# Optimization experiments

Measured on AMD Instinct MI355X. Metric: run time of the kernel, lower is better.

Reference implementation:

```python
import jax, jax.numpy as jnp
import numpy as np

N_CHILDS = 50000
N_EDGES = 500000
NODE_FEAT = 256
NUM_SEM = 57
HID = 256
EDGE_FEAT = 64
EDGE_TYPES = 4
NUM_ITERS = 2


def setup_inputs() -> dict:
    key = jax.random.key(0)
    ks = jax.random.split(key, 12)
    d_in = NODE_FEAT + NUM_SEM            # 313
    d_ne = 2 * HID + EDGE_FEAT + EDGE_TYPES  # 580
    d_par = HID * (NUM_ITERS + 1)         # 768
    def lin(k, fan_in, fan_out):
        kw, kb = jax.random.split(k)
        s = 1.0 / np.sqrt(fan_in)
        return (jax.random.uniform(kw, (fan_in, fan_out), jnp.float32, -s, s),
                jax.random.uniform(kb, (fan_out,), jnp.float32, -s, s))
    W_child, b_child = lin(ks[0], d_in, HID)
    W_ne0, b_ne0 = lin(ks[1], d_ne, HID)
    W_ne1, b_ne1 = lin(ks[2], d_ne, HID)
    W_parent, b_parent = lin(ks[3], d_par, NODE_FEAT)
    return {
        "child_feats": jax.random.normal(ks[4], (1, N_CHILDS, d_in), jnp.float32),
        "child_exists": jnp.ones((1, N_CHILDS, 1), jnp.float32),
        "edge_type_onehot": jax.random.normal(ks[5], (1, N_EDGES, EDGE_TYPES), jnp.float32),
        "edge_feats": jax.random.normal(ks[6], (1, N_EDGES, EDGE_FEAT), jnp.float32),
        "edge_indices": jax.random.randint(ks[7], (1, N_EDGES, 2), 0, N_CHILDS, jnp.int64),
        "W_child": W_child, "b_child": b_child,
        "W_ne0": W_ne0, "b_ne0": b_ne0,
        "W_ne1": W_ne1, "b_ne1": b_ne1,
        "W_parent": W_parent, "b_parent": b_parent,
    }


def reference(child_feats, child_exists, edge_type_onehot, edge_feats, edge_indices,
              W_child, b_child, W_ne0, b_ne0, W_ne1, b_ne1, W_parent, b_parent):
    n = child_feats.shape[1]
    # node embedding: linear + relu, mask non-existent children
    x = jax.nn.relu(jnp.einsum('bnd,dh->bnh', child_feats, W_child) + b_child)
    x = x * child_exists                              # [1, N, H]
    iter_parent = [x.max(axis=1)]                     # symmetric_type == 'max'
    ef = jnp.concatenate([edge_type_onehot, edge_feats], axis=2)[0]  # [E, 4+64]
    src = edge_indices[0, :, 0]
    dst = edge_indices[0, :, 1]
    cnt = jax.ops.segment_sum(jnp.ones((src.shape[0],), x.dtype), src, num_segments=n)
    denom = jnp.maximum(cnt, 1.0)[:, None]            # scatter_mean clamp
    for W, b in ((W_ne0, b_ne0), (W_ne1, b_ne1)):
        nef = jnp.concatenate([x[0, src], x[0, dst], ef], axis=1)  # [E, 580]
        nef = jax.nn.relu(nef @ W + b)                # [E, H]
        # edge_symmetric_type == 'avg': scatter_mean over source index
        x = (jax.ops.segment_sum(nef, src, num_segments=n) / denom)[None]
        iter_parent.append(x.max(axis=1))
    parent = jnp.concatenate(iter_parent, axis=1)     # [1, H*(iters+1)]
    return jax.nn.relu(parent @ W_parent + b_parent)  # [1, node_feat_size]
```

## Files before the change

### kernel.cpp

```cpp
#include <hip/hip_runtime.h>

#define NC   50000
#define NE   500000
#define DIN  313
#define DNE  580
#define KPC  320
#define KB   96
#define NB_SCAN 196

typedef __attribute__((ext_vector_type(8))) short bf16x8;
typedef __attribute__((ext_vector_type(4))) float f32x4;

static __device__ __forceinline__ unsigned short f2bf(float f) {
    unsigned u = __float_as_uint(f);
    unsigned r = (u + 0x7fff + ((u >> 16) & 1)) >> 16;
    return (unsigned short)r;
}
static __device__ __forceinline__ float bf2f(unsigned short u) {
    return __uint_as_float(((unsigned)u) << 16);
}
static __device__ __forceinline__ void gload_lds16(const unsigned short* g, unsigned short* l) {
    __builtin_amdgcn_global_load_lds(
        (const __attribute__((address_space(1))) unsigned int*)(g),
        (__attribute__((address_space(3))) unsigned int*)(l), 16, 0, 0);
}

__global__ __launch_bounds__(256) void prep_w_kernel(
    const float* __restrict__ W0, const float* __restrict__ W1,
    const float* __restrict__ Wc,
    unsigned short* __restrict__ Wpt, unsigned short* __restrict__ Wbt,
    unsigned short* __restrict__ Wct)
{
    int b = blockIdx.x;
    if (b < 1024) {
        int layer = b >> 9, n2 = b & 511;
        const float* W = layer ? W1 : W0;
        unsigned short* dst = Wpt + (size_t)layer * 512 * 256 + (size_t)n2 * 256;
        int t = threadIdx.x;
        int ch = t >> 5, s = (t >> 3) & 3, j = t & 7;
        int gk = ch * 32 + ((s ^ (n2 & 3)) * 8) + j;
        float v = (n2 < 256) ? W[(size_t)gk * 256 + n2] : W[(size_t)(256 + gk) * 256 + (n2 - 256)];
        dst[t] = f2bf(v);
    } else if (b < 1536) {
        int idx = b - 1024;
        int layer = idx >> 8, n = idx & 255;
        const float* W = layer ? W1 : W0;
        unsigned short* dst = Wbt + (size_t)layer * 256 * KB + (size_t)n * KB;
        int t = threadIdx.x;
        if (t < KB) {
            float v = (512 + t < DNE) ? W[(size_t)(512 + t) * 256 + n] : 0.0f;
            dst[t] = f2bf(v);
        }
    } else {
        int n = b - 1536;
        unsigned short* dst = Wct + (size_t)n * KPC;
        for (int t = threadIdx.x; t < KPC; t += 256) {
            int ch = t >> 5, s = (t >> 3) & 3, j = t & 7;
            int gk = ch * 32 + ((s ^ (n & 3)) * 8) + j;
            float v = (gk < DIN) ? Wc[(size_t)gk * 256 + n] : 0.0f;
            dst[t] = f2bf(v);
        }
    }
}

__global__ __launch_bounds__(256, 4) void child_mfma_kernel(
    const float* __restrict__ cf, const float* __restrict__ exists,
    const unsigned short* __restrict__ Wct, const float* __restrict__ bias,
    unsigned short* __restrict__ xb, float* __restrict__ pmax)
{
    __shared__ unsigned short sA[64][40];
    __shared__ unsigned short sB[256][32];
    __shared__ float smax[256];

    const int tid = threadIdx.x, lane = tid & 63, wid = tid >> 6;
    const int wm = wid >> 1, wn = wid & 1, l15 = lane & 15, l4 = lane >> 4;
    const int node0 = blockIdx.x * 64;
    const int arow = tid >> 2, s3 = tid & 3;

    smax[tid] = 0.0f;

    f32x4 acc[2][8];
    #pragma unroll
    for (int mi = 0; mi < 2; ++mi)
        #pragma unroll
        for (int ni = 0; ni < 8; ++ni)
            acc[mi][ni] = (f32x4){0.f, 0.f, 0.f, 0.f};

    int nodeA = node0 + arow; if (nodeA >= NC) nodeA = NC - 1;

    for (int ch = 0; ch < 10; ++ch) {
        #pragma unroll
        for (int i = 0; i < 4; ++i) {
            int n = (wid << 6) + (i << 4) + (lane >> 2);
            gload_lds16(Wct + (size_t)n * KPC + ch * 32 + (lane & 3) * 8,
                        &sB[(wid << 6) + (i << 4)][0]);
        }
        {
            int gk0 = ch * 32 + s3 * 8;
            union { unsigned short u[8]; int4 v; } pk;
            #pragma unroll
            for (int j = 0; j < 8; ++j) {
                int gk = gk0 + j;
                float f = (gk < DIN) ? cf[(size_t)nodeA * DIN + gk] : 0.0f;
                pk.u[j] = f2bf(f);
            }
            *(int4*)&sA[arow][s3 * 8] = pk.v;
        }
        __syncthreads();
        bf16x8 af[2];
        #pragma unroll
        for (int mi = 0; mi < 2; ++mi)
            af[mi] = *(const bf16x8*)&sA[wm * 32 + mi * 16 + l15][l4 * 8];
        #pragma unroll
        for (int ni = 0; ni < 8; ++ni) {
            int n = wn * 128 + ni * 16 + l15;
            bf16x8 bfr = *(const bf16x8*)&sB[n][(l4 ^ (n & 3)) * 8];
            acc[0][ni] = __builtin_amdgcn_mfma_f32_16x16x32_bf16(af[0], bfr, acc[0][ni], 0, 0, 0);
            acc[1][ni] = __builtin_amdgcn_mfma_f32_16x16x32_bf16(af[1], bfr, acc[1][ni], 0, 0, 0);
        }
        __syncthreads();
    }

    float bv[8];
    #pragma unroll
    for (int ni = 0; ni < 8; ++ni) bv[ni] = bias[wn * 128 + ni * 16 + l15];
    float cmax[8];
    #pragma unroll
    for (int ni = 0; ni < 8; ++ni) cmax[ni] = 0.0f;

    #pragma unroll
    for (int mi = 0; mi < 2; ++mi) {
        #pragma unroll
        for (int r = 0; r < 4; ++r) {
            int node = node0 + wm * 32 + mi * 16 + l4 * 4 + r;
            if (node < NC) {
                float ex = exists[node];
                #pragma unroll
                for (int ni = 0; ni < 8; ++ni) {
                    float v = fmaxf(acc[mi][ni][r] + bv[ni], 0.f) * ex;
                    xb[(size_t)node * 256 + wn * 128 + ni * 16 + l15] = f2bf(v);
                    cmax[ni] = fmaxf(cmax[ni], v);
                }
            }
        }
    }
    #pragma unroll
    for (int ni = 0; ni < 8; ++ni)
        atomicMax((unsigned int*)&smax[wn * 128 + ni * 16 + l15], __float_as_uint(cmax[ni]));
    __syncthreads();
    atomicMax((unsigned int*)&pmax[tid], __float_as_uint(smax[tid]));
}

__global__ __launch_bounds__(256, 3) void node_gemm_kernel(
    const unsigned short* __restrict__ xb,
    const unsigned short* __restrict__ Wpt,
    unsigned short* __restrict__ yp)
{
    __shared__ unsigned short sA[2][64][40];
    __shared__ unsigned short sB[2][256][32];

    const int tid = threadIdx.x, lane = tid & 63, wid = tid >> 6;
    const int wm = wid >> 1, wn = wid & 1, l15 = lane & 15, l4 = lane >> 4;
    const int node0 = blockIdx.x * 64;
    const int n0 = blockIdx.y * 256;
    const int arow = tid >> 2, s3 = tid & 3;

    int nodeA = node0 + arow; if (nodeA >= NC) nodeA = NC - 1;

    f32x4 acc[2][8];
    #pragma unroll
    for (int mi = 0; mi < 2; ++mi)
        #pragma unroll
        for (int ni = 0; ni < 8; ++ni)
            acc[mi][ni] = (f32x4){0.f, 0.f, 0.f, 0.f};

    #pragma unroll
    for (int i = 0; i < 4; ++i) {
        int n = (wid << 6) + (i << 4) + (lane >> 2);
        gload_lds16(Wpt + (size_t)(n0 + n) * 256 + (lane & 3) * 8, &sB[0][(wid << 6) + (i << 4)][0]);
    }
    *(int4*)&sA[0][arow][s3 * 8] = *(const int4*)(xb + (size_t)nodeA * 256 + s3 * 8);
    __syncthreads();

    int buf = 0;
    for (int ch = 0; ch < 8; ++ch) {
        const int nch = ch + 1;
        int4 areg;
        if (nch < 8) {
            #pragma unroll
            for (int i = 0; i < 4; ++i) {
                int n = (wid << 6) + (i << 4) + (lane >> 2);
                gload_lds16(Wpt + (size_t)(n0 + n) * 256 + nch * 32 + (lane & 3) * 8,
                            &sB[buf ^ 1][(wid << 6) + (i << 4)][0]);
            }
            areg = *(const int4*)(xb + (size_t)nodeA * 256 + nch * 32 + s3 * 8);
        }
        bf16x8 af[2];
        #pragma unroll
        for (int mi = 0; mi < 2; ++mi)
            af[mi] = *(const bf16x8*)&sA[buf][wm * 32 + mi * 16 + l15][l4 * 8];
        #pragma unroll
        for (int ni = 0; ni < 8; ++ni) {
            int n = wn * 128 + ni * 16 + l15;
            bf16x8 bfr = *(const bf16x8*)&sB[buf][n][(l4 ^ (n & 3)) * 8];
            acc[0][ni] = __builtin_amdgcn_mfma_f32_16x16x32_bf16(af[0], bfr, acc[0][ni], 0, 0, 0);
            acc[1][ni] = __builtin_amdgcn_mfma_f32_16x16x32_bf16(af[1], bfr, acc[1][ni], 0, 0, 0);
        }
        if (nch < 8) *(int4*)&sA[buf ^ 1][arow][s3 * 8] = areg;
        __syncthreads();
        buf ^= 1;
    }

    #pragma unroll
    for (int mi = 0; mi < 2; ++mi) {
        #pragma unroll
        for (int r = 0; r < 4; ++r) {
            int node = node0 + wm * 32 + mi * 16 + l4 * 4 + r;
            if (node < NC) {
                #pragma unroll
                for (int ni = 0; ni < 8; ++ni)
                    yp[(size_t)node * 512 + n0 + wn * 128 + ni * 16 + l15] = f2bf(acc[mi][ni][r]);
            }
        }
    }
}

__global__ __launch_bounds__(256) void count_int_kernel(
    const int* __restrict__ eidx, int* __restrict__ icnt)
{
    int t = blockIdx.x * 256 + threadIdx.x;
    if (t < NE) atomicAdd(&icnt[eidx[2 * t]], 1);
}

__global__ __launch_bounds__(256) void scan1_kernel(
    const int* __restrict__ icnt, int* __restrict__ part)
{
    __shared__ int sd[256];
    int i = blockIdx.x * 256 + threadIdx.x;
    sd[threadIdx.x] = (i < NC) ? icnt[i] : 0;
    __syncthreads();
    for (int d = 128; d > 0; d >>= 1) {
        if (threadIdx.x < d) sd[threadIdx.x] += sd[threadIdx.x + d];
        __syncthreads();
    }
    if (threadIdx.x == 0) part[blockIdx.x] = sd[0];
}

__global__ void scan2_kernel(int* __restrict__ part)
{
    if (threadIdx.x == 0) {
        int acc = 0;
        for (int i = 0; i < NB_SCAN; ++i) { int v = part[i]; part[i] = acc; acc += v; }
    }
}

__global__ __launch_bounds__(256) void scan3_kernel(
    const int* __restrict__ icnt, const int* __restrict__ part,
    int* __restrict__ cur)
{
    __shared__ int sc[256];
    const int t = threadIdx.x;
    int i = blockIdx.x * 256 + t;
    int val = (i < NC) ? icnt[i] : 0;
    sc[t] = val;
    __syncthreads();
    for (int d = 1; d < 256; d <<= 1) {
        int x = (t >= d) ? sc[t - d] : 0;
        __syncthreads();
        sc[t] += x;
        __syncthreads();
    }
    if (i < NC) cur[i] = part[blockIdx.x] + sc[t] - val;
}

__global__ __launch_bounds__(256) void bin_kernel(
    const int* __restrict__ eidx, int* __restrict__ cur, int* __restrict__ perm)
{
    int t = blockIdx.x * 256 + threadIdx.x;
    if (t < NE) {
        int s = eidx[2 * t];
        int p = atomicAdd(&cur[s], 1);
        perm[p] = t;
    }
}

__global__ __launch_bounds__(256) void inv_kernel(
    const int* __restrict__ icnt, float* __restrict__ inv)
{
    int t = blockIdx.x * 256 + threadIdx.x;
    if (t < NC) inv[t] = 1.0f / fmaxf((float)icnt[t], 1.0f);
}

__global__ __launch_bounds__(256, 4) void combine_kernel(
    const unsigned short* __restrict__ yp,
    const float* __restrict__ eto, const float* __restrict__ efe,
    const int* __restrict__ eidx, const int* __restrict__ perm,
    const unsigned short* __restrict__ Wbt,
    const float* __restrict__ bias,
    float* __restrict__ accb)
{
    __shared__ __align__(16) unsigned char smemraw[16 * 258 * 4];
    unsigned short (*sA)[64][40] = (unsigned short (*)[64][40])smemraw;
    float (*ep)[258] = (float (*)[258])smemraw;
    __shared__ int s_src[64], s_dst[64], s_perm[64];

    const int tid = threadIdx.x;
    const int nwg = gridDim.x;
    const int q = nwg >> 3, rr = nwg & 7;
    const int xcd = blockIdx.x & 7, within = blockIdx.x >> 3;
    const int bid = (xcd < rr ? xcd * (q + 1) : rr * (q + 1) + (xcd - rr) * q) + within;
    const int e0 = bid * 64;

    if (tid < 64) {
        int ee = e0 + tid; if (ee >= NE) ee = NE - 1;
        int e = perm[ee];
        s_perm[tid] = e;
        s_src[tid] = eidx[2 * e];
        s_dst[tid] = eidx[2 * e + 1];
    }
    const int lane = tid & 63;
    const int wid  = tid >> 6;
    const int wm   = wid >> 1;
    const int wn   = wid & 1;
    const int l15  = lane & 15;
    const int l4   = lane >> 4;
    const int arow = tid >> 2;
    const int s3   = tid & 3;

    __syncthreads();

    const int my_e = s_perm[arow];
    #pragma unroll
    for (int ch = 0; ch < 3; ++ch) {
        int g0 = ch * 32 + s3 * 8;
        union { unsigned short u[8]; int4 v; } pk;
        #pragma unroll
        for (int j = 0; j < 8; ++j) {
            int g = g0 + j;
            float f = 0.0f;
            if (g < 4)       f = eto[(size_t)my_e * 4 + g];
            else if (g < 68) f = efe[(size_t)my_e * 64 + (g - 4)];
            pk.u[j] = f2bf(f);
        }
        *(int4*)&sA[ch][arow][s3 * 8] = pk.v;
    }
    __syncthreads();

    f32x4 acc[2][8];
    #pragma unroll
    for (int mi = 0; mi < 2; ++mi)
        #pragma unroll
        for (int ni = 0; ni < 8; ++ni)
            acc[mi][ni] = (f32x4){0.f, 0.f, 0.f, 0.f};

    const unsigned short* wp = Wbt + (size_t)(wn * 128 + l15) * KB + l4 * 8;
    #pragma unroll
    for (int ch = 0; ch < 3; ++ch) {
        bf16x8 bw[8];
        #pragma unroll
        for (int ni = 0; ni < 8; ++ni)
            bw[ni] = *(const bf16x8*)(wp + (size_t)ni * 16 * KB + ch * 32);
        bf16x8 af0 = *(const bf16x8*)&sA[ch][wm * 32 + l15][l4 * 8];
        bf16x8 af1 = *(const bf16x8*)&sA[ch][wm * 32 + 16 + l15][l4 * 8];
        #pragma unroll
        for (int ni = 0; ni < 8; ++ni) {
            acc[0][ni] = __builtin_amdgcn_mfma_f32_16x16x32_bf16(af0, bw[ni], acc[0][ni], 0, 0, 0);
            acc[1][ni] = __builtin_amdgcn_mfma_f32_16x16x32_bf16(af1, bw[ni], acc[1][ni], 0, 0, 0);
        }
    }
    __syncthreads();

    const int col = tid;
    const float b_col = bias[col];

    int curn = s_src[0];
    int rstart = 0;
    float run = 0.f;
    #pragma unroll
    for (int c = 0; c < 4; ++c) {
        if (wm == (c >> 1)) {
            const int mi = c & 1;
            #pragma unroll
            for (int ni = 0; ni < 8; ++ni) {
                #pragma unroll
                for (int r = 0; r < 4; ++r)
                    ep[l4 * 4 + r][wn * 128 + ni * 16 + l15] = acc[mi][ni][r];
            }
        }
        float yt[16], ym[16];
        #pragma unroll
        for (int r = 0; r < 16; ++r) {
            int row = c * 16 + r;
            yt[r] = bf2f(yp[(size_t)s_src[row] * 512 + col]);
            ym[r] = bf2f(yp[(size_t)s_dst[row] * 512 + 256 + col]);
        }
        __syncthreads();
        #pragma unroll
        for (int r = 0; r < 16; ++r) {
            int row = c * 16 + r;
            float v = 0.0f;
            if (e0 + row < NE)
                v = fmaxf(ep[r][col] + yt[r] + ym[r] + b_col, 0.f);
            int sr = s_src[row];
            if (sr != curn) {
                if (rstart > 0) accb[(size_t)curn * 256 + col] = run;
                else            atomicAdd(&accb[(size_t)curn * 256 + col], run);
                curn = sr; run = v; rstart = row;
            } else {
                run += v;
            }
        }
        __syncthreads();
    }
    atomicAdd(&accb[(size_t)curn * 256 + col], run);
}

__global__ __launch_bounds__(256) void finalize_kernel(
    const float* __restrict__ src, const float* __restrict__ inv,
    unsigned short* __restrict__ xb_out, float* __restrict__ pmax, int n)
{
    const int tid = threadIdx.x;
    int i0 = blockIdx.x * 128;
    int iend = i0 + 128; if (iend > n) iend = n;
    float m = 0.0f;
    for (int i = i0; i < iend; ++i) {
        float v = src[(size_t)i * 256 + tid];
        v *= inv[i];
        xb_out[(size_t)i * 256 + tid] = f2bf(v);
        m = fmaxf(m, v);
    }
    atomicMax((unsigned int*)&pmax[tid], __float_as_uint(m));
}

__global__ __launch_bounds__(256) void parent_kernel(
    const float* __restrict__ pmax, const float* __restrict__ W,
    const float* __restrict__ bias, float* __restrict__ out)
{
    __shared__ float sp[768];
    const int tid = threadIdx.x;
    for (int i = tid; i < 768; i += 256) sp[i] = pmax[i];
    __syncthreads();
    float s = bias[tid];
    for (int k = 0; k < 768; ++k) s = fmaf(sp[k], W[(size_t)k * 256 + tid], s);
    out[tid] = fmaxf(s, 0.f);
}

extern "C" void kernel_launch(void* const* d_in, const int* in_sizes, int n_in,
                              void* d_out, int out_size, void* d_ws, size_t ws_size,
                              hipStream_t stream)
{
    const float* cf   = (const float*)d_in[0];
    const float* ex   = (const float*)d_in[1];
    const float* eto  = (const float*)d_in[2];
    const float* efe  = (const float*)d_in[3];
    const int*   eidx = (const int*)d_in[4];
    const float* Wc   = (const float*)d_in[5];
    const float* bc   = (const float*)d_in[6];
    const float* W0   = (const float*)d_in[7];
    const float* b0   = (const float*)d_in[8];
    const float* W1   = (const float*)d_in[9];
    const float* b1   = (const float*)d_in[10];
    const float* Wp   = (const float*)d_in[11];
    const float* bp   = (const float*)d_in[12];

    float*          accb = (float*)d_ws;
    float*          invv = accb + (size_t)NC * 256;
    float*          pmax = invv + NC;
    unsigned short* xb   = (unsigned short*)(pmax + 768);
    unsigned short* yp   = xb + (size_t)NC * 256;
    unsigned short* Wpt  = yp + (size_t)NC * 512;
    unsigned short* Wbt  = Wpt + (size_t)2 * 512 * 256;
    unsigned short* Wct  = Wbt + (size_t)2 * 256 * KB;
    int*            icnt = (int*)(Wct + (size_t)256 * KPC);
    int*            part = icnt + NC;
    int*            curb = part + 256;
    int*            perm = curb + NC;

    hipMemsetAsync(pmax, 0, 768 * sizeof(float), stream);
    hipMemsetAsync(icnt, 0, NC * sizeof(int), stream);

    prep_w_kernel<<<1792, 256, 0, stream>>>(W0, W1, Wc, Wpt, Wbt, Wct);
    child_mfma_kernel<<<(NC + 63) / 64, 256, 0, stream>>>(cf, ex, Wct, bc, xb, pmax);

    count_int_kernel<<<(NE + 255) / 256, 256, 0, stream>>>(eidx, icnt);
    scan1_kernel<<<NB_SCAN, 256, 0, stream>>>(icnt, part);
    scan2_kernel<<<1, 64, 0, stream>>>(part);
    scan3_kernel<<<NB_SCAN, 256, 0, stream>>>(icnt, part, curb);
    bin_kernel<<<(NE + 255) / 256, 256, 0, stream>>>(eidx, curb, perm);
    inv_kernel<<<(NC + 255) / 256, 256, 0, stream>>>(icnt, invv);

    for (int it = 0; it < 2; ++it) {
        node_gemm_kernel<<<dim3((NC + 63) / 64, 2), 256, 0, stream>>>(
            xb, Wpt + (size_t)it * 512 * 256, yp);
        hipMemsetAsync(accb, 0, (size_t)NC * 256 * sizeof(float), stream);
        combine_kernel<<<(NE + 63) / 64, 256, 0, stream>>>(
            yp, eto, efe, eidx, perm, Wbt + (size_t)it * 256 * KB, it ? b1 : b0, accb);
        finalize_kernel<<<(NC + 127) / 128, 256, 0, stream>>>(accb, invv, xb, pmax + 256 * (it + 1), NC);
    }
    parent_kernel<<<1, 256, 0, stream>>>(pmax, Wp, bp, (float*)d_out);
}
```

Baseline: 720.8 us.

## Fuse edge combine with node finalize using node-partitioned CSR segments

Edges are now processed per block of 32 destination nodes using CSR offsets, so each block owns complete segments. It can divide by the count and write bf16 node features directly, which removes the fp32 accumulator, its memset, the atomics and the separate finalize kernel. Edge features are precomputed once into sorted, bf16-packed arrays that are loaded with direct-to-LDS loads. The cost is uneven work per block from variable degrees and a serial tile loop per block.

```diff
diff --git a/kernel.cpp b/kernel.cpp
--- a/kernel.cpp
+++ b/kernel.cpp
@@ -2,10 +2,12 @@
 
 #define NC   50000
 #define NE   500000
+#define NEP  (NE + 64)
 #define DIN  313
 #define DNE  580
 #define KPC  320
 #define KB   96
+#define NPB  32
 #define NB_SCAN 196
 
 typedef __attribute__((ext_vector_type(8))) short bf16x8;
@@ -256,7 +258,7 @@
 
 __global__ __launch_bounds__(256) void scan3_kernel(
     const int* __restrict__ icnt, const int* __restrict__ part,
-    int* __restrict__ cur)
+    int* __restrict__ cur, int* __restrict__ soff)
 {
     __shared__ int sc[256];
     const int t = threadIdx.x;
@@ -270,7 +272,11 @@
         sc[t] += x;
         __syncthreads();
     }
-    if (i < NC) cur[i] = part[blockIdx.x] + sc[t] - val;
+    if (i < NC) {
+        int start = part[blockIdx.x] + sc[t] - val;
+        cur[i]  = start;
+        soff[i] = start;
+    }
 }
 
 __global__ __launch_bounds__(256) void bin_kernel(
@@ -285,151 +291,194 @@
 }
 
 __global__ __launch_bounds__(256) void inv_kernel(
-    const int* __restrict__ icnt, float* __restrict__ inv)
+    const int* __restrict__ icnt, float* __restrict__ inv, int* __restrict__ soff)
 {
     int t = blockIdx.x * 256 + threadIdx.x;
     if (t < NC) inv[t] = 1.0f / fmaxf((float)icnt[t], 1.0f);
-}
-
-__global__ __launch_bounds__(256, 4) void combine_kernel(
+    if (blockIdx.x == 0 && threadIdx.x == 0) soff[NC] = NE;
+}
+
+__global__ __launch_bounds__(256) void ef_prep_kernel(
+    const float* __restrict__ eto, const float* __restrict__ efe,
+    const int* __restrict__ perm, const int* __restrict__ eidx,
+    unsigned short* __restrict__ efc01, unsigned short* __restrict__ efc2,
+    int* __restrict__ esrc, int* __restrict__ edst)
+{
+    int p = blockIdx.x * 256 + threadIdx.x;
+    if (p >= NE) return;
+    int e = perm[p];
+    esrc[p] = eidx[2 * e];
+    edst[p] = eidx[2 * e + 1];
+    const float* efr = efe + (size_t)e * 64;
+
+    union { unsigned short u[8]; int4 v; } pk;
+    {
+        float4 a = *(const float4*)(eto + (size_t)e * 4);
+        float4 b = *(const float4*)(efr + 0);
+        pk.u[0]=f2bf(a.x); pk.u[1]=f2bf(a.y); pk.u[2]=f2bf(a.z); pk.u[3]=f2bf(a.w);
+        pk.u[4]=f2bf(b.x); pk.u[5]=f2bf(b.y); pk.u[6]=f2bf(b.z); pk.u[7]=f2bf(b.w);
+        *(int4*)(efc01 + (size_t)p * 32) = pk.v;
+    }
+    #pragma unroll
+    for (int g = 1; g < 4; ++g) {
+        float4 a = *(const float4*)(efr + g * 8 - 4);
+        float4 b = *(const float4*)(efr + g * 8);
+        pk.u[0]=f2bf(a.x); pk.u[1]=f2bf(a.y); pk.u[2]=f2bf(a.z); pk.u[3]=f2bf(a.w);
+        pk.u[4]=f2bf(b.x); pk.u[5]=f2bf(b.y); pk.u[6]=f2bf(b.z); pk.u[7]=f2bf(b.w);
+        *(int4*)(efc01 + (size_t)p * 32 + g * 8) = pk.v;
+    }
+    #pragma unroll
+    for (int g = 0; g < 4; ++g) {
+        float4 a = *(const float4*)(efr + 28 + g * 8);
+        float4 b = *(const float4*)(efr + 32 + g * 8);
+        pk.u[0]=f2bf(a.x); pk.u[1]=f2bf(a.y); pk.u[2]=f2bf(a.z); pk.u[3]=f2bf(a.w);
+        pk.u[4]=f2bf(b.x); pk.u[5]=f2bf(b.y); pk.u[6]=f2bf(b.z); pk.u[7]=f2bf(b.w);
+        *(int4*)(efc01 + ((size_t)NEP + p) * 32 + g * 8) = pk.v;
+    }
+    {
+        float4 a = *(const float4*)(efr + 60);
+        pk.u[0]=f2bf(a.x); pk.u[1]=f2bf(a.y); pk.u[2]=f2bf(a.z); pk.u[3]=f2bf(a.w);
+        pk.u[4]=0; pk.u[5]=0; pk.u[6]=0; pk.u[7]=0;
+        *(int4*)(efc2 + (size_t)p * 8) = pk.v;
+    }
+}
+
+__global__ __launch_bounds__(256, 4) void combine_node_kernel(
     const unsigned short* __restrict__ yp,
-    const float* __restrict__ eto, const float* __restrict__ efe,
-    const int* __restrict__ eidx, const int* __restrict__ perm,
+    const unsigned short* __restrict__ efc01,
+    const unsigned short* __restrict__ efc2,
+    const int* __restrict__ esrc, const int* __restrict__ edst,
+    const int* __restrict__ soff, const float* __restrict__ invv,
     const unsigned short* __restrict__ Wbt,
     const float* __restrict__ bias,
-    float* __restrict__ accb)
-{
-    __shared__ __align__(16) unsigned char smemraw[16 * 258 * 4];
-    unsigned short (*sA)[64][40] = (unsigned short (*)[64][40])smemraw;
-    float (*ep)[258] = (float (*)[258])smemraw;
-    __shared__ int s_src[64], s_dst[64], s_perm[64];
+    unsigned short* __restrict__ xb_out, float* __restrict__ pmax)
+{
+    __shared__ unsigned short sA[2][64][32];
+    __shared__ unsigned short sA2[64][8];
+    __shared__ float ep[16][258];
+    __shared__ int s_src[64], s_dst[64];
+    __shared__ float s_inv[NPB];
+    __shared__ int s_offa[NPB + 1];
 
     const int tid = threadIdx.x;
-    const int nwg = gridDim.x;
-    const int q = nwg >> 3, rr = nwg & 7;
-    const int xcd = blockIdx.x & 7, within = blockIdx.x >> 3;
-    const int bid = (xcd < rr ? xcd * (q + 1) : rr * (q + 1) + (xcd - rr) * q) + within;
-    const int e0 = bid * 64;
-
-    if (tid < 64) {
-        int ee = e0 + tid; if (ee >= NE) ee = NE - 1;
-        int e = perm[ee];
-        s_perm[tid] = e;
-        s_src[tid] = eidx[2 * e];
-        s_dst[tid] = eidx[2 * e + 1];
-    }
-    const int lane = tid & 63;
-    const int wid  = tid >> 6;
-    const int wm   = wid >> 1;
-    const int wn   = wid & 1;
-    const int l15  = lane & 15;
-    const int l4   = lane >> 4;
-    const int arow = tid >> 2;
-    const int s3   = tid & 3;
-
+    const int n0 = blockIdx.x * NPB;
+    if (tid < NPB) {
+        int n = n0 + tid;
+        s_inv[tid] = invv[n < NC ? n : NC - 1];
+    }
+    if (tid <= NPB) {
+        int n = n0 + tid;
+        s_offa[tid] = soff[n < NC ? n : NC];
+    }
     __syncthreads();
-
-    const int my_e = s_perm[arow];
-    #pragma unroll
-    for (int ch = 0; ch < 3; ++ch) {
-        int g0 = ch * 32 + s3 * 8;
-        union { unsigned short u[8]; int4 v; } pk;
-        #pragma unroll
-        for (int j = 0; j < 8; ++j) {
-            int g = g0 + j;
-            float f = 0.0f;
-            if (g < 4)       f = eto[(size_t)my_e * 4 + g];
-            else if (g < 68) f = efe[(size_t)my_e * 64 + (g - 4)];
-            pk.u[j] = f2bf(f);
-        }
-        *(int4*)&sA[ch][arow][s3 * 8] = pk.v;
-    }
-    __syncthreads();
-
-    f32x4 acc[2][8];
-    #pragma unroll
-    for (int mi = 0; mi < 2; ++mi)
-        #pragma unroll
-        for (int ni = 0; ni < 8; ++ni)
-            acc[mi][ni] = (f32x4){0.f, 0.f, 0.f, 0.f};
-
-    const unsigned short* wp = Wbt + (size_t)(wn * 128 + l15) * KB + l4 * 8;
-    #pragma unroll
-    for (int ch = 0; ch < 3; ++ch) {
-        bf16x8 bw[8];
-        #pragma unroll
-        for (int ni = 0; ni < 8; ++ni)
-            bw[ni] = *(const bf16x8*)(wp + (size_t)ni * 16 * KB + ch * 32);
-        bf16x8 af0 = *(const bf16x8*)&sA[ch][wm * 32 + l15][l4 * 8];
-        bf16x8 af1 = *(const bf16x8*)&sA[ch][wm * 32 + 16 + l15][l4 * 8];
-        #pragma unroll
-        for (int ni = 0; ni < 8; ++ni) {
-            acc[0][ni] = __builtin_amdgcn_mfma_f32_16x16x32_bf16(af0, bw[ni], acc[0][ni], 0, 0, 0);
-            acc[1][ni] = __builtin_amdgcn_mfma_f32_16x16x32_bf16(af1, bw[ni], acc[1][ni], 0, 0, 0);
-        }
-    }
-    __syncthreads();
-
+    const int S = s_offa[0], E = s_offa[NPB];
+
+    const int lane = tid & 63, wid = tid >> 6;
+    const int wm = wid >> 1, wn = wid & 1;
+    const int l15 = lane & 15, l4 = lane >> 4;
     const int col = tid;
     const float b_col = bias[col];
-
-    int curn = s_src[0];
-    int rstart = 0;
+    const unsigned short* wp = Wbt + (size_t)(wn * 128 + l15) * KB + l4 * 8;
+
+    int curn = -1;
     float run = 0.f;
-    #pragma unroll
-    for (int c = 0; c < 4; ++c) {
-        if (wm == (c >> 1)) {
-            const int mi = c & 1;
+    float colmax = 0.f;
+
+    const int nT = (E - S + 63) >> 6;
+    for (int t = 0; t < nT; ++t) {
+        const int eS = S + t * 64;
+        if (tid < 64) {
+            int e = eS + tid; if (e > NE - 1) e = NE - 1;
+            s_src[tid] = esrc[e];
+            s_dst[tid] = edst[e];
+        }
+        gload_lds16(efc01 + ((size_t)eS + wid * 16) * 32 + lane * 8, &sA[0][wid * 16][0]);
+        gload_lds16(efc01 + ((size_t)NEP + eS + wid * 16) * 32 + lane * 8, &sA[1][wid * 16][0]);
+        if (wid == 0)
+            gload_lds16(efc2 + (size_t)eS * 8 + lane * 8, &sA2[0][0]);
+        __syncthreads();
+
+        f32x4 acc[2][8];
+        #pragma unroll
+        for (int mi = 0; mi < 2; ++mi)
+            #pragma unroll
+            for (int ni = 0; ni < 8; ++ni)
+                acc[mi][ni] = (f32x4){0.f, 0.f, 0.f, 0.f};
+
+        #pragma unroll
+        for (int ch = 0; ch < 3; ++ch) {
+            bf16x8 bw[8];
+            #pragma unroll
+            for (int ni = 0; ni < 8; ++ni)
+                bw[ni] = *(const bf16x8*)(wp + (size_t)ni * 16 * KB + ch * 32);
+            bf16x8 af0, af1;
+            if (ch < 2) {
+                af0 = *(const bf16x8*)&sA[ch][wm * 32 + l15][l4 * 8];
+                af1 = *(const bf16x8*)&sA[ch][wm * 32 + 16 + l15][l4 * 8];
+            } else {
+                bf16x8 z = (bf16x8){0,0,0,0,0,0,0,0};
+                bf16x8 a0 = *(const bf16x8*)&sA2[wm * 32 + l15][0];
+                bf16x8 a1 = *(const bf16x8*)&sA2[wm * 32 + 16 + l15][0];
+                af0 = (l4 == 0) ? a0 : z;
+                af1 = (l4 == 0) ? a1 : z;
+            }
             #pragma unroll
             for (int ni = 0; ni < 8; ++ni) {
+                acc[0][ni] = __builtin_amdgcn_mfma_f32_16x16x32_bf16(af0, bw[ni], acc[0][ni], 0, 0, 0);
+                acc[1][ni] = __builtin_amdgcn_mfma_f32_16x16x32_bf16(af1, bw[ni], acc[1][ni], 0, 0, 0);
+            }
+        }
+
+        #pragma unroll
+        for (int c = 0; c < 4; ++c) {
+            if (wm == (c >> 1)) {
+                const int mi = c & 1;
                 #pragma unroll
-                for (int r = 0; r < 4; ++r)
-                    ep[l4 * 4 + r][wn * 128 + ni * 16 + l15] = acc[mi][ni][r];
-            }
-        }
-        float yt[16], ym[16];
-        #pragma unroll
-        for (int r = 0; r < 16; ++r) {
-            int row = c * 16 + r;
-            yt[r] = bf2f(yp[(size_t)s_src[row] * 512 + col]);
-            ym[r] = bf2f(yp[(size_t)s_dst[row] * 512 + 256 + col]);
-        }
-        __syncthreads();
-        #pragma unroll
-        for (int r = 0; r < 16; ++r) {
-            int row = c * 16 + r;
-            float v = 0.0f;
-            if (e0 + row < NE)
-                v = fmaxf(ep[r][col] + yt[r] + ym[r] + b_col, 0.f);
-            int sr = s_src[row];
-            if (sr != curn) {
-                if (rstart > 0) accb[(size_t)curn * 256 + col] = run;
-                else            atomicAdd(&accb[(size_t)curn * 256 + col], run);
-                curn = sr; run = v; rstart = row;
-            } else {
-                run += v;
-            }
-        }
-        __syncthreads();
-    }
-    atomicAdd(&accb[(size_t)curn * 256 + col], run);
-}
-
-__global__ __launch_bounds__(256) void finalize_kernel(
-    const float* __restrict__ src, const float* __restrict__ inv,
-    unsigned short* __restrict__ xb_out, float* __restrict__ pmax, int n)
-{
-    const int tid = threadIdx.x;
-    int i0 = blockIdx.x * 128;
-    int iend = i0 + 128; if (iend > n) iend = n;
-    float m = 0.0f;
-    for (int i = i0; i < iend; ++i) {
-        float v = src[(size_t)i * 256 + tid];
-        v *= inv[i];
-        xb_out[(size_t)i * 256 + tid] = f2bf(v);
-        m = fmaxf(m, v);
-    }
-    atomicMax((unsigned int*)&pmax[tid], __float_as_uint(m));
+                for (int ni = 0; ni < 8; ++ni) {
+                    #pragma unroll
+                    for (int r = 0; r < 4; ++r)
+                        ep[l4 * 4 + r][wn * 128 + ni * 16 + l15] = acc[mi][ni][r];
+                }
+            }
+            float yt[16], ym[16];
+            #pragma unroll
+            for (int r = 0; r < 16; ++r) {
+                int row = c * 16 + r;
+                yt[r] = bf2f(yp[(size_t)s_src[row] * 512 + col]);
+                ym[r] = bf2f(yp[(size_t)s_dst[row] * 512 + 256 + col]);
+            }
+            __syncthreads();
+            #pragma unroll
+            for (int r = 0; r < 16; ++r) {
+                int row = c * 16 + r;
+                bool valid = (eS + row) < E;
+                float v = valid ? fmaxf(ep[r][col] + yt[r] + ym[r] + b_col, 0.f) : 0.f;
+                int sr = valid ? s_src[row] : curn;
+                if (sr != curn) {
+                    if (curn >= 0) {
+                        float o = run * s_inv[curn - n0];
+                        xb_out[(size_t)curn * 256 + col] = f2bf(o);
+                        colmax = fmaxf(colmax, o);
+                    }
+                    curn = sr; run = v;
+                } else {
+                    run += v;
+                }
+            }
+            __syncthreads();
+        }
+    }
+    if (curn >= 0) {
+        float o = run * s_inv[curn - n0];
+        xb_out[(size_t)curn * 256 + col] = f2bf(o);
+        colmax = fmaxf(colmax, o);
+    }
+    for (int i = 0; i < NPB; ++i) {
+        int n = n0 + i;
+        if (n < NC && s_offa[i] == s_offa[i + 1])
+            xb_out[(size_t)n * 256 + col] = 0;
+    }
+    atomicMax((unsigned int*)&pmax[col], __float_as_uint(colmax));
 }
 
 __global__ __launch_bounds__(256) void parent_kernel(
@@ -463,18 +512,22 @@
     const float* Wp   = (const float*)d_in[11];
     const float* bp   = (const float*)d_in[12];
 
-    float*          accb = (float*)d_ws;
-    float*          invv = accb + (size_t)NC * 256;
-    float*          pmax = invv + NC;
-    unsigned short* xb   = (unsigned short*)(pmax + 768);
-    unsigned short* yp   = xb + (size_t)NC * 256;
-    unsigned short* Wpt  = yp + (size_t)NC * 512;
-    unsigned short* Wbt  = Wpt + (size_t)2 * 512 * 256;
-    unsigned short* Wct  = Wbt + (size_t)2 * 256 * KB;
-    int*            icnt = (int*)(Wct + (size_t)256 * KPC);
-    int*            part = icnt + NC;
-    int*            curb = part + 256;
-    int*            perm = curb + NC;
+    float*          invv  = (float*)d_ws;
+    float*          pmax  = invv + NC;
+    unsigned short* xb    = (unsigned short*)(pmax + 768);
+    unsigned short* yp    = xb + (size_t)NC * 256;
+    unsigned short* Wpt   = yp + (size_t)NC * 512;
+    unsigned short* Wbt   = Wpt + (size_t)2 * 512 * 256;
+    unsigned short* Wct   = Wbt + (size_t)2 * 256 * KB;
+    unsigned short* efc01 = Wct + (size_t)256 * KPC;
+    unsigned short* efc2  = efc01 + (size_t)2 * NEP * 32;
+    int*            icnt  = (int*)(efc2 + (size_t)NEP * 8);
+    int*            part  = icnt + NC;
+    int*            curb  = part + 256;
+    int*            soff  = curb + NC;
+    int*            perm  = soff + NC + 1;
+    int*            esrc  = perm + NE;
+    int*            edst  = esrc + NE;
 
     hipMemsetAsync(pmax, 0, 768 * sizeof(float), stream);
     hipMemsetAsync(icnt, 0, NC * sizeof(int), stream);
@@ -485,17 +538,18 @@
     count_int_kernel<<<(NE + 255) / 256, 256, 0, stream>>>(eidx, icnt);
     scan1_kernel<<<NB_SCAN, 256, 0, stream>>>(icnt, part);
     scan2_kernel<<<1, 64, 0, stream>>>(part);
-    scan3_kernel<<<NB_SCAN, 256, 0, stream>>>(icnt, part, curb);
+    scan3_kernel<<<NB_SCAN, 256, 0, stream>>>(icnt, part, curb, soff);
     bin_kernel<<<(NE + 255) / 256, 256, 0, stream>>>(eidx, curb, perm);
-    inv_kernel<<<(NC + 255) / 256, 256, 0, stream>>>(icnt, invv);
+    inv_kernel<<<(NC + 255) / 256, 256, 0, stream>>>(icnt, invv, soff);
+    ef_prep_kernel<<<(NE + 255) / 256, 256, 0, stream>>>(eto, efe, perm, eidx, efc01, efc2, esrc, edst);
 
     for (int it = 0; it < 2; ++it) {
         node_gemm_kernel<<<dim3((NC + 63) / 64, 2), 256, 0, stream>>>(
             xb, Wpt + (size_t)it * 512 * 256, yp);
-        hipMemsetAsync(accb, 0, (size_t)NC * 256 * sizeof(float), stream);
-        combine_kernel<<<(NE + 63) / 64, 256, 0, stream>>>(
-            yp, eto, efe, eidx, perm, Wbt + (size_t)it * 256 * KB, it ? b1 : b0, accb);
-        finalize_kernel<<<(NC + 127) / 128, 256, 0, stream>>>(accb, invv, xb, pmax + 256 * (it + 1), NC);
+        combine_node_kernel<<<(NC + NPB - 1) / NPB, 256, 0, stream>>>(
+            yp, efc01, efc2, esrc, edst, soff, invv,
+            Wbt + (size_t)it * 256 * KB, it ? b1 : b0,
+            xb, pmax + 256 * (it + 1));
     }
     parent_kernel<<<1, 256, 0, stream>>>(pmax, Wp, bp, (float*)d_out);
 }
```

Result: slower. 903.8 us (+25.4%).
